# Kernel tuning notes

Measured on AMD Instinct MI355X. Metric: run time of the kernel, lower is better.

Reference implementation:

```python
import jax, jax.numpy as jnp
import numpy as np

B, L, H, F = 8, 1024, 512, 4

def setup_inputs() -> dict:
    key = jax.random.key(0)
    ks = jax.random.split(key, 5)
    x = jax.random.normal(ks[0], (B, L, H), dtype=jnp.float32)
    x_mask = jax.random.randint(ks[1], (B, L), 0, 2).astype(jnp.int32)
    W_proj = jax.random.normal(ks[2], (H, H * F), dtype=jnp.float32) * (1.0 / np.sqrt(H))
    b_proj = jnp.zeros((H * F,), dtype=jnp.float32)
    W_gate = jax.random.normal(ks[3], (2 * H, 2 * H), dtype=jnp.float32) * (1.0 / np.sqrt(2 * H))
    b_gate = jnp.zeros((2 * H,), dtype=jnp.float32)
    return {"x": x, "x_mask": x_mask, "W_proj": W_proj, "b_proj": b_proj,
            "W_gate": W_gate, "b_gate": b_gate}

def masked_softmax(logits, mask, eps=1e-13):
    # allennlp-style masked softmax used throughout sgnlp:
    # softmax(logits * mask) * mask, renormalized.
    m = mask.astype(logits.dtype)
    p = jax.nn.softmax(logits * m, axis=-1) * m
    return p / (p.sum(axis=-1, keepdims=True) + eps)

def reference(x, x_mask, W_proj, b_proj, W_gate, b_gate):
    b, l, h = x.shape
    # multi-factor projection: (B,L,H) -> (B,L,H,F) with relu (Linear activation='relu', dropout=0)
    y = jax.nn.relu(jnp.einsum('blh,hk->blk', x, W_proj) + b_proj)
    y = y.reshape(b, l, h, F)
    # per-factor self-attn scores stacked on last axis: (B,L,L,F)
    scores = jnp.einsum('blhf,bmhf->blmf', y, y)
    self_attn = scores.max(axis=-1)  # attn_pooling == 'max'
    # pairwise mask, zero diagonal
    mask = x_mask[:, :, None] * x_mask[:, None, :]
    mask = mask * (1 - jnp.eye(l, dtype=mask.dtype))
    alpha = masked_softmax(self_attn, mask)
    multi_attn_enc = jnp.einsum('blm,bmh->blh', alpha, x)
    joint = jnp.concatenate([x, multi_attn_enc], axis=-1)  # (B,L,2H)
    gate = jax.nn.sigmoid(jnp.einsum('blk,kj->blj', joint, W_gate) + b_gate)
    return gate * joint
```

## Files before the change

### kernel.cpp

```cpp
#include <hip/hip_runtime.h>


typedef _Float16 half8 __attribute__((ext_vector_type(8)));
typedef float floatx4 __attribute__((ext_vector_type(4)));

typedef const __attribute__((address_space(1))) void* gas_ptr;
typedef __attribute__((address_space(3))) void* las_ptr;


template<int NCH, int NT>
__device__ __forceinline__ void init_ptrs(const _Float16* src, int row0, int ld,
                                          const _Float16* gp[NCH]) {
  int t = threadIdx.x;
#pragma unroll
  for (int p = 0; p < NCH; ++p) {
    int c = p * NT + t;
    int row = c >> 3;
    int kg = c & 7;
    int gk = (kg ^ (row & 7)) << 3;
    gp[p] = src + (size_t)(row0 + row) * ld + gk;
  }
}

template<int NCH, int NT>
__device__ __forceinline__ void stage(const _Float16* const gp[NCH], _Float16* ldsbuf) {
  int t = threadIdx.x;
#pragma unroll
  for (int p = 0; p < NCH; ++p)
    __builtin_amdgcn_global_load_lds((gas_ptr)gp[p],
                                     (las_ptr)(ldsbuf + t * 8 + p * NT * 8), 16, 0, 0);
}

template<int NCH>
__device__ __forceinline__ void bump(const _Float16* gp[NCH], int d) {
#pragma unroll
  for (int p = 0; p < NCH; ++p) gp[p] += d;
}

__device__ __forceinline__ half8 frag_ld(const _Float16* lds, int row, int g) {
  return *(const half8*)(lds + row * 64 + ((g ^ (row & 7)) << 3));
}

__device__ __forceinline__ void mfma_tile44(const _Float16* lds_a, const _Float16* lds_b,
                                            floatx4 acc[4][4], int wm, int wn,
                                            int l16, int quad) {
#pragma unroll
  for (int kf = 0; kf < 2; ++kf) {
    half8 af[4], bf[4];
#pragma unroll
    for (int i = 0; i < 4; ++i) af[i] = frag_ld(lds_a, wm * 64 + i * 16 + l16, kf * 4 + quad);
#pragma unroll
    for (int i = 0; i < 4; ++i) bf[i] = frag_ld(lds_b, wn * 64 + i * 16 + l16, kf * 4 + quad);
#pragma unroll
    for (int mi = 0; mi < 4; ++mi)
#pragma unroll
      for (int ni = 0; ni < 4; ++ni)
        acc[mi][ni] = __builtin_amdgcn_mfma_f32_16x16x32_f16(af[mi], bf[ni], acc[mi][ni], 0, 0, 0);
  }
}

#define ZERO_ACC44(acc)                                 \
  _Pragma("unroll") for (int mi = 0; mi < 4; ++mi)      \
  _Pragma("unroll") for (int ni = 0; ni < 4; ++ni)      \
  _Pragma("unroll") for (int r = 0; r < 4; ++r) acc[mi][ni][r] = 0.0f;

__device__ __forceinline__ void mfma_tile42(const _Float16* la, const _Float16* lb,
                                            floatx4 acc[4][2], int wm, int wn,
                                            int l16, int quad) {
#pragma unroll
  for (int kf = 0; kf < 2; ++kf) {
    half8 af[4], bf[2];
#pragma unroll
    for (int i = 0; i < 4; ++i) af[i] = frag_ld(la, wm * 64 + i * 16 + l16, kf * 4 + quad);
#pragma unroll
    for (int i = 0; i < 2; ++i) bf[i] = frag_ld(lb, wn * 32 + i * 16 + l16, kf * 4 + quad);
#pragma unroll
    for (int mi = 0; mi < 4; ++mi)
#pragma unroll
      for (int ni = 0; ni < 2; ++ni)
        acc[mi][ni] = __builtin_amdgcn_mfma_f32_16x16x32_f16(af[mi], bf[ni], acc[mi][ni], 0, 0, 0);
  }
}

#define ZERO_ACC42(acc)                                 \
  _Pragma("unroll") for (int mi = 0; mi < 4; ++mi)      \
  _Pragma("unroll") for (int ni = 0; ni < 2; ++ni)      \
  _Pragma("unroll") for (int r = 0; r < 4; ++r) acc[mi][ni][r] = 0.0f;


__global__ __launch_bounds__(256) void prep_kernel(const float* __restrict__ xin,
                                                   _Float16* __restrict__ x16,
                                                   _Float16* __restrict__ xT,
                                                   const float* __restrict__ Wp,
                                                   _Float16* __restrict__ WpT,
                                                   const float* __restrict__ Wg,
                                                   _Float16* __restrict__ WgT) {
  __shared__ float tile[32][33];
  int id = blockIdx.x;
  int tx = threadIdx.x & 31, ty = threadIdx.x >> 5;
  if (id < 4096) {
    const int R = 1024, C = 512;
    int b = id & 7, rest = id >> 3;
    int c0 = (rest & 15) * 32, r0 = (rest >> 4) * 32;
    size_t boff = (size_t)b * R * C;
    const float* in = xin + boff;
    _Float16* o16 = x16 + boff;
    _Float16* oT = xT + boff;
#pragma unroll
    for (int i = 0; i < 32; i += 8) {
      float v = in[(size_t)(r0 + ty + i) * C + c0 + tx];
      tile[ty + i][tx] = v;
      o16[(size_t)(r0 + ty + i) * C + c0 + tx] = (_Float16)v;
    }
    __syncthreads();
#pragma unroll
    for (int i = 0; i < 32; i += 8)
      oT[(size_t)(c0 + ty + i) * R + r0 + tx] = (_Float16)tile[tx][ty + i];
  } else {
    int w = id - 4096;
    int bx = w & 63, by = (w >> 6) & 15, bz = w >> 10;
    const float* in; _Float16* out; int R, C, c0, r0;
    if (bz == 0) {
      in = Wp; out = WpT; R = 512; C = 2048;
      c0 = bx * 32; r0 = by * 32;
    } else {
      in = Wg; out = WgT; R = 1024; C = 1024;
      c0 = (bx & 31) * 32; r0 = (by * 2 + (bx >> 5)) * 32;
    }
#pragma unroll
    for (int i = 0; i < 32; i += 8)
      tile[ty + i][tx] = in[(size_t)(r0 + ty + i) * C + c0 + tx];
    __syncthreads();
#pragma unroll
    for (int i = 0; i < 32; i += 8) {
      int rr = c0 + ty + i;
      int prow = (bz == 0) ? ((rr & 3) * 512 + (rr >> 2)) : rr;
      out[(size_t)prow * R + r0 + tx] = (_Float16)tile[tx][ty + i];
    }
  }
}


__global__ __launch_bounds__(256) void proj_kernel(const _Float16* __restrict__ x16,
                                                   const _Float16* __restrict__ WpT,
                                                   const float* __restrict__ bp,
                                                   _Float16* __restrict__ y_t) {
  __shared__ __align__(16) _Float16 ldsA[2][128 * 64];
  __shared__ __align__(16) _Float16 ldsB[2][128 * 64];
  int i0 = blockIdx.x * 128, n0 = blockIdx.y * 128;
  int t = threadIdx.x, lane = t & 63, w = t >> 6;
  int wm = w >> 1, wn = w & 1, quad = lane >> 4, l16 = lane & 15;
  const _Float16* gpA[4]; const _Float16* gpB[4];
  init_ptrs<4, 256>(x16, i0, 512, gpA);
  init_ptrs<4, 256>(WpT, n0, 512, gpB);
  floatx4 acc[4][4];
  ZERO_ACC44(acc);
  stage<4, 256>(gpA, ldsA[0]); bump<4>(gpA, 64);
  stage<4, 256>(gpB, ldsB[0]); bump<4>(gpB, 64);
#pragma unroll 1
  for (int kt = 0; kt < 8; ++kt) {
    __syncthreads();
    if (kt < 7) {
      stage<4, 256>(gpA, ldsA[(kt + 1) & 1]); bump<4>(gpA, 64);
      stage<4, 256>(gpB, ldsB[(kt + 1) & 1]); bump<4>(gpB, 64);
    }
    mfma_tile44(ldsA[kt & 1], ldsB[kt & 1], acc, wm, wn, l16, quad);
  }
#pragma unroll
  for (int mi = 0; mi < 4; ++mi)
#pragma unroll
    for (int ni = 0; ni < 4; ++ni)
#pragma unroll
      for (int r = 0; r < 4; ++r) {
        int gr = i0 + wm * 64 + mi * 16 + quad * 4 + r;
        int gc = n0 + wn * 64 + ni * 16 + l16;
        int f = gc >> 9, h = gc & 511;
        float c = fmaxf(acc[mi][ni][r] + bp[h * 4 + f], 0.0f);
        int b = gr >> 10, l = gr & 1023;
        y_t[(((size_t)(b * 4 + f)) * 1024 + l) * 512 + h] = (_Float16)c;
      }
}


__global__ __launch_bounds__(256, 3) void score_kernel(const _Float16* __restrict__ y_t,
                                                       float* __restrict__ S) {
  __shared__ __align__(16) char smem[49152];
  _Float16* LA0 = (_Float16*)smem;
  _Float16* LA1 = (_Float16*)(smem + 16384);
  _Float16* LB0 = (_Float16*)(smem + 32768);
  _Float16* LB1 = (_Float16*)(smem + 40960);
  int id = blockIdx.x;
  int b = id & 7;
  int tt = id >> 3;
  int ti = 0;
  while (tt >= 16 - 2 * ti) { tt -= 16 - 2 * ti; ++ti; }
  int jh = 2 * ti + tt;
  int i0 = ti * 128, j0 = jh * 64;
  int t = threadIdx.x, lane = t & 63, w = t >> 6;
  int wm = w >> 1, wn = w & 1, quad = lane >> 4, l16 = lane & 15;
  const int PLANE = 1024 * 512;
  const _Float16* base = y_t + (size_t)b * 4 * PLANE;
  const _Float16* gpA[4]; const _Float16* gpB[2];
  init_ptrs<4, 256>(base, i0, 512, gpA);
  init_ptrs<2, 256>(base, j0, 512, gpB);
  floatx4 acc[4][2], smax[4][2];
  ZERO_ACC42(acc);
  stage<4, 256>(gpA, LA0); bump<4>(gpA, 64);
  stage<2, 256>(gpB, LB0); bump<2>(gpB, 64);
#pragma unroll 1
  for (int f = 0; f < 4; ++f) {
#pragma unroll 1
    for (int kt = 0; kt < 8; ++kt) {
      __syncthreads();
      if (f * 8 + kt < 31) {
        if (kt == 7) { bump<4>(gpA, PLANE - 512); bump<2>(gpB, PLANE - 512); }
        stage<4, 256>(gpA, ((kt + 1) & 1) ? LA1 : LA0); bump<4>(gpA, 64);
        stage<2, 256>(gpB, ((kt + 1) & 1) ? LB1 : LB0); bump<2>(gpB, 64);
      }
      mfma_tile42((kt & 1) ? LA1 : LA0, (kt & 1) ? LB1 : LB0, acc, wm, wn, l16, quad);
    }
    if (f == 0) {
#pragma unroll
      for (int mi = 0; mi < 4; ++mi)
#pragma unroll
        for (int ni = 0; ni < 2; ++ni) smax[mi][ni] = acc[mi][ni];
    } else {
#pragma unroll
      for (int mi = 0; mi < 4; ++mi)
#pragma unroll
        for (int ni = 0; ni < 2; ++ni)
#pragma unroll
          for (int r = 0; r < 4; ++r)
            smax[mi][ni][r] = fmaxf(smax[mi][ni][r], acc[mi][ni][r]);
    }
    ZERO_ACC42(acc);
  }
  float* Sb = S + (size_t)b * 1024 * 1024;
#pragma unroll
  for (int mi = 0; mi < 4; ++mi)
#pragma unroll
    for (int ni = 0; ni < 2; ++ni)
#pragma unroll
      for (int r = 0; r < 4; ++r) {
        int gi = i0 + wm * 64 + mi * 16 + quad * 4 + r;
        int gj = j0 + wn * 32 + ni * 16 + l16;
        Sb[(size_t)gi * 1024 + gj] = smax[mi][ni][r];
      }
  if (jh >= 2 * ti + 2) {
    __syncthreads();
    float* tl = (float*)smem;
#pragma unroll
    for (int mi = 0; mi < 4; ++mi)
#pragma unroll
      for (int ni = 0; ni < 2; ++ni)
#pragma unroll
        for (int r = 0; r < 4; ++r)
          tl[(wm * 64 + mi * 16 + quad * 4 + r) * 65 + (wn * 32 + ni * 16 + l16)] =
              smax[mi][ni][r];
    __syncthreads();
#pragma unroll 1
    for (int k = 0; k < 32; ++k) {
      int flat = k * 256 + t;
      int rm = flat >> 7, cm = flat & 127;
      Sb[(size_t)(j0 + rm) * 1024 + (i0 + cm)] = tl[cm * 65 + rm];
    }
  }
}


__global__ __launch_bounds__(256) void softmax_kernel(const float* __restrict__ S,
                                                      const int* __restrict__ xmask,
                                                      _Float16* __restrict__ alpha) {
  __shared__ float red[16];
  int row = blockIdx.x;
  int b = row >> 10, l = row & 1023;
  const float* sr = S + (size_t)row * 1024;
  const int* mr = xmask + b * 1024;
  int t = threadIdx.x, lane = t & 63, wid = t >> 6;
  int rm = mr[l];
  float v[4], mm[4];
  float vmax = 0.0f;
#pragma unroll
  for (int q = 0; q < 4; ++q) {
    int i = t + q * 256;
    int m = (rm && mr[i] && (i != l)) ? 1 : 0;
    mm[q] = (float)m;
    v[q] = m ? sr[i] : 0.0f;
    vmax = fmaxf(vmax, v[q]);
  }
  for (int off = 32; off; off >>= 1) vmax = fmaxf(vmax, __shfl_down(vmax, off));
  if (lane == 0) red[wid] = vmax;
  __syncthreads();
  if (t == 0) red[8] = fmaxf(fmaxf(red[0], red[1]), fmaxf(red[2], red[3]));
  __syncthreads();
  vmax = red[8];
  float e[4], E = 0.0f, E2 = 0.0f;
#pragma unroll
  for (int q = 0; q < 4; ++q) {
    e[q] = expf(v[q] - vmax);
    E += e[q];
    E2 += e[q] * mm[q];
  }
  for (int off = 32; off; off >>= 1) {
    E += __shfl_down(E, off);
    E2 += __shfl_down(E2, off);
  }
  if (lane == 0) { red[wid] = E; red[4 + wid] = E2; }
  __syncthreads();
  if (t == 0) {
    red[9] = red[0] + red[1] + red[2] + red[3];
    red[10] = red[4] + red[5] + red[6] + red[7];
  }
  __syncthreads();
  E = red[9]; E2 = red[10];
  float inv = 1.0f / (E2 + 1e-13f * E);
  _Float16* ar = alpha + (size_t)row * 1024;
#pragma unroll
  for (int q = 0; q < 4; ++q) {
    int i = t + q * 256;
    ar[i] = (_Float16)(e[q] * mm[q] * inv);
  }
}


__global__ __launch_bounds__(256) void attn_kernel(const _Float16* __restrict__ alpha,
                                                   const _Float16* __restrict__ xT,
                                                   _Float16* __restrict__ enc) {
  __shared__ __align__(16) _Float16 ldsA[2][64 * 64];
  __shared__ __align__(16) _Float16 ldsB[2][128 * 64];
  int id = blockIdx.x;
  int b = id & 7;
  int r2 = id >> 3;
  int i0 = (r2 >> 2) * 64;
  int n0 = (r2 & 3) * 128;
  const _Float16* A = alpha + (size_t)b * 1024 * 1024;
  const _Float16* Bm = xT + (size_t)b * 512 * 1024;
  int t = threadIdx.x, lane = t & 63, wn = t >> 6;
  int quad = lane >> 4, l16 = lane & 15;
  const _Float16* gpA[2]; const _Float16* gpB[4];
  init_ptrs<2, 256>(A, i0, 1024, gpA);
  init_ptrs<4, 256>(Bm, n0, 1024, gpB);
  floatx4 acc[4][2];
  ZERO_ACC42(acc);
  stage<2, 256>(gpA, ldsA[0]); bump<2>(gpA, 64);
  stage<4, 256>(gpB, ldsB[0]); bump<4>(gpB, 64);
#pragma unroll 1
  for (int kt = 0; kt < 16; ++kt) {
    __syncthreads();
    if (kt < 15) {
      stage<2, 256>(gpA, ldsA[(kt + 1) & 1]); bump<2>(gpA, 64);
      stage<4, 256>(gpB, ldsB[(kt + 1) & 1]); bump<4>(gpB, 64);
    }
    const _Float16* la = ldsA[kt & 1];
    const _Float16* lb = ldsB[kt & 1];
#pragma unroll
    for (int kf = 0; kf < 2; ++kf) {
      half8 af[4], bf[2];
#pragma unroll
      for (int i = 0; i < 4; ++i) af[i] = frag_ld(la, i * 16 + l16, kf * 4 + quad);
#pragma unroll
      for (int i = 0; i < 2; ++i) bf[i] = frag_ld(lb, wn * 32 + i * 16 + l16, kf * 4 + quad);
#pragma unroll
      for (int mi = 0; mi < 4; ++mi)
#pragma unroll
        for (int ni = 0; ni < 2; ++ni)
          acc[mi][ni] = __builtin_amdgcn_mfma_f32_16x16x32_f16(af[mi], bf[ni], acc[mi][ni], 0, 0, 0);
    }
  }
  _Float16* eb = enc + (size_t)b * 1024 * 512;
#pragma unroll
  for (int mi = 0; mi < 4; ++mi)
#pragma unroll
    for (int ni = 0; ni < 2; ++ni)
#pragma unroll
      for (int r = 0; r < 4; ++r) {
        int gr = i0 + mi * 16 + quad * 4 + r;
        int gc = n0 + wn * 32 + ni * 16 + l16;
        eb[(size_t)gr * 512 + gc] = (_Float16)acc[mi][ni][r];
      }
}


__global__ __launch_bounds__(256) void gate_kernel(const _Float16* __restrict__ x16,
                                                   const _Float16* __restrict__ enc,
                                                   const _Float16* __restrict__ WgT,
                                                   const float* __restrict__ bg,
                                                   float* __restrict__ out) {
  __shared__ __align__(16) _Float16 ldsA[2][128 * 64];
  __shared__ __align__(16) _Float16 ldsB[2][128 * 64];
  int i0 = blockIdx.x * 128, n0 = blockIdx.y * 128;
  int t = threadIdx.x, lane = t & 63, w = t >> 6;
  int wm = w >> 1, wn = w & 1, quad = lane >> 4, l16 = lane & 15;
  const _Float16* gpA[4]; const _Float16* gpA2[4]; const _Float16* gpB[4];
  init_ptrs<4, 256>(x16, i0, 512, gpA);
  init_ptrs<4, 256>(enc, i0, 512, gpA2);
  init_ptrs<4, 256>(WgT, n0, 1024, gpB);
  floatx4 acc[4][4];
  ZERO_ACC44(acc);
  stage<4, 256>(gpA, ldsA[0]); bump<4>(gpA, 64);
  stage<4, 256>(gpB, ldsB[0]); bump<4>(gpB, 64);
#pragma unroll 1
  for (int kt = 0; kt < 16; ++kt) {
    __syncthreads();
    if (kt < 15) {
      if (kt < 7) { stage<4, 256>(gpA,  ldsA[(kt + 1) & 1]); bump<4>(gpA, 64); }
      else        { stage<4, 256>(gpA2, ldsA[(kt + 1) & 1]); bump<4>(gpA2, 64); }
      stage<4, 256>(gpB, ldsB[(kt + 1) & 1]); bump<4>(gpB, 64);
    }
    mfma_tile44(ldsA[kt & 1], ldsB[kt & 1], acc, wm, wn, l16, quad);
  }
#pragma unroll
  for (int mi = 0; mi < 4; ++mi)
#pragma unroll
    for (int ni = 0; ni < 4; ++ni)
#pragma unroll
      for (int r = 0; r < 4; ++r) {
        int gr = i0 + wm * 64 + mi * 16 + quad * 4 + r;
        int gc = n0 + wn * 64 + ni * 16 + l16;
        float c = acc[mi][ni][r] + bg[gc];
        float g = 1.0f / (1.0f + expf(-c));
        float jv = (gc < 512) ? (float)x16[(size_t)gr * 512 + gc]
                              : (float)enc[(size_t)gr * 512 + (gc - 512)];
        out[(size_t)gr * 1024 + gc] = g * jv;
      }
}


extern "C" void kernel_launch(void* const* d_in, const int* in_sizes, int n_in,
                              void* d_out, int out_size, void* d_ws, size_t ws_size,
                              hipStream_t stream) {
  const float* x  = (const float*)d_in[0];
  const int* xm   = (const int*)d_in[1];
  const float* Wp = (const float*)d_in[2];
  const float* bp = (const float*)d_in[3];
  const float* Wg = (const float*)d_in[4];
  const float* bg = (const float*)d_in[5];
  float* out = (float*)d_out;

  char* ws = (char*)d_ws;
  const size_t MB = 1024 * 1024;
  _Float16* x16 = (_Float16*)(ws);
  _Float16* xT  = (_Float16*)(ws + 8 * MB);
  _Float16* WpT = (_Float16*)(ws + 16 * MB);
  _Float16* WgT = (_Float16*)(ws + 18 * MB);
  _Float16* y_t = (_Float16*)(ws + 20 * MB);
  float*    S   = (float*)(ws + 52 * MB);
  _Float16* alpha = (_Float16*)(ws + 20 * MB);
  _Float16* enc   = (_Float16*)(ws + 36 * MB);

  prep_kernel<<<6144, 256, 0, stream>>>(x, x16, xT, Wp, WpT, Wg, WgT);

  proj_kernel<<<dim3(64, 16), 256, 0, stream>>>(x16, WpT, bp, y_t);
  score_kernel<<<576, 256, 0, stream>>>(y_t, S);
  softmax_kernel<<<8192, 256, 0, stream>>>(S, xm, alpha);
  attn_kernel<<<512, 256, 0, stream>>>(alpha, xT, enc);
  gate_kernel<<<dim3(64, 8), 256, 0, stream>>>(x16, enc, WgT, bg, out);
}
```

Baseline: 198.9 us.

## Fuse masked softmax into attention GEMM, keeping alpha rows in LDS

Merges the softmax and attention kernels into one. Each 512-thread block computes a 32-row strip of alpha in LDS (one wave per row, wave-level reductions), then multiplies it by xT, with B fragments read directly from global memory in a register double buffer. This removes the fp16 alpha round-trip through global memory and one launch. The cost is a grid of only 256 large blocks with heavy LDS use, so occupancy is lower. B fragments are also loaded uncoalesced from global without LDS staging.

Measured after the change: 206.9 us. 1.04x slower.

```diff
diff --git a/kernel.cpp b/kernel.cpp
--- a/kernel.cpp
+++ b/kernel.cpp
@@ -2,6 +2,7 @@
 
 
 typedef _Float16 half8 __attribute__((ext_vector_type(8)));
+typedef _Float16 half4v __attribute__((ext_vector_type(4)));
 typedef float floatx4 __attribute__((ext_vector_type(4)));
 
 typedef const __attribute__((address_space(1))) void* gas_ptr;
@@ -268,114 +269,115 @@
 }
 
 
-__global__ __launch_bounds__(256) void softmax_kernel(const float* __restrict__ S,
-                                                      const int* __restrict__ xmask,
-                                                      _Float16* __restrict__ alpha) {
-  __shared__ float red[16];
-  int row = blockIdx.x;
-  int b = row >> 10, l = row & 1023;
-  const float* sr = S + (size_t)row * 1024;
-  const int* mr = xmask + b * 1024;
-  int t = threadIdx.x, lane = t & 63, wid = t >> 6;
-  int rm = mr[l];
-  float v[4], mm[4];
-  float vmax = 0.0f;
-#pragma unroll
-  for (int q = 0; q < 4; ++q) {
-    int i = t + q * 256;
-    int m = (rm && mr[i] && (i != l)) ? 1 : 0;
-    mm[q] = (float)m;
-    v[q] = m ? sr[i] : 0.0f;
-    vmax = fmaxf(vmax, v[q]);
-  }
-  for (int off = 32; off; off >>= 1) vmax = fmaxf(vmax, __shfl_down(vmax, off));
-  if (lane == 0) red[wid] = vmax;
+__global__ __launch_bounds__(512) void smattn_kernel(const float* __restrict__ S,
+                                                     const int* __restrict__ xmask,
+                                                     const _Float16* __restrict__ xT,
+                                                     _Float16* __restrict__ enc) {
+  __shared__ __align__(16) _Float16 lal[16 * 2048];
+  __shared__ float lm[1024];
+  int id = blockIdx.x;
+  int b = id & 7, it = id >> 3;
+  int i0 = it * 32;
+  int t = threadIdx.x, lane = t & 63, w = t >> 6;
+  lm[t] = (float)xmask[b * 1024 + t];
+  lm[t + 512] = (float)xmask[b * 1024 + t + 512];
   __syncthreads();
-  if (t == 0) red[8] = fmaxf(fmaxf(red[0], red[1]), fmaxf(red[2], red[3]));
+  const float* Sb = S + ((size_t)b * 1024 + i0) * 1024;
+#pragma unroll 1
+  for (int rr = 0; rr < 4; ++rr) {
+    int r = w * 4 + rr;
+    int grow = i0 + r;
+    float rmv = lm[grow];
+    const float* sr = Sb + (size_t)r * 1024;
+    float e[16], mk[16];
+    float vmax = 0.0f;
+#pragma unroll
+    for (int q = 0; q < 4; ++q) {
+      float4 sv = *(const float4*)(sr + q * 256 + lane * 4);
+#pragma unroll
+      for (int u = 0; u < 4; ++u) {
+        int j = q * 256 + lane * 4 + u;
+        float m = (rmv != 0.0f && lm[j] != 0.0f && j != grow) ? 1.0f : 0.0f;
+        float v = m * ((const float*)&sv)[u];
+        mk[q * 4 + u] = m;
+        e[q * 4 + u] = v;
+        vmax = fmaxf(vmax, v);
+      }
+    }
+#pragma unroll
+    for (int off = 32; off; off >>= 1) vmax = fmaxf(vmax, __shfl_xor(vmax, off));
+    float E = 0.0f, E2 = 0.0f;
+#pragma unroll
+    for (int i = 0; i < 16; ++i) {
+      e[i] = expf(e[i] - vmax);
+      E += e[i];
+      E2 += e[i] * mk[i];
+    }
+#pragma unroll
+    for (int off = 32; off; off >>= 1) {
+      E += __shfl_xor(E, off);
+      E2 += __shfl_xor(E2, off);
+    }
+    float inv = 1.0f / (E2 + 1e-13f * E);
+#pragma unroll
+    for (int q = 0; q < 4; ++q) {
+      int kt = q * 4 + (lane >> 4);
+      int jg = (lane >> 1) & 7;
+      int off8 = (lane & 1) * 4;
+      half4v hv;
+#pragma unroll
+      for (int u = 0; u < 4; ++u) hv[u] = (_Float16)(e[q * 4 + u] * mk[q * 4 + u] * inv);
+      *(half4v*)(&lal[kt * 2048 + r * 64 + ((jg ^ (r & 7)) << 3) + off8]) = hv;
+    }
+  }
   __syncthreads();
-  vmax = red[8];
-  float e[4], E = 0.0f, E2 = 0.0f;
-#pragma unroll
-  for (int q = 0; q < 4; ++q) {
-    e[q] = expf(v[q] - vmax);
-    E += e[q];
-    E2 += e[q] * mm[q];
-  }
-  for (int off = 32; off; off >>= 1) {
-    E += __shfl_down(E, off);
-    E2 += __shfl_down(E2, off);
-  }
-  if (lane == 0) { red[wid] = E; red[4 + wid] = E2; }
-  __syncthreads();
-  if (t == 0) {
-    red[9] = red[0] + red[1] + red[2] + red[3];
-    red[10] = red[4] + red[5] + red[6] + red[7];
-  }
-  __syncthreads();
-  E = red[9]; E2 = red[10];
-  float inv = 1.0f / (E2 + 1e-13f * E);
-  _Float16* ar = alpha + (size_t)row * 1024;
-#pragma unroll
-  for (int q = 0; q < 4; ++q) {
-    int i = t + q * 256;
-    ar[i] = (_Float16)(e[q] * mm[q] * inv);
-  }
-}
-
-
-__global__ __launch_bounds__(256) void attn_kernel(const _Float16* __restrict__ alpha,
-                                                   const _Float16* __restrict__ xT,
-                                                   _Float16* __restrict__ enc) {
-  __shared__ __align__(16) _Float16 ldsA[2][64 * 64];
-  __shared__ __align__(16) _Float16 ldsB[2][128 * 64];
-  int id = blockIdx.x;
-  int b = id & 7;
-  int r2 = id >> 3;
-  int i0 = (r2 >> 2) * 64;
-  int n0 = (r2 & 3) * 128;
-  const _Float16* A = alpha + (size_t)b * 1024 * 1024;
-  const _Float16* Bm = xT + (size_t)b * 512 * 1024;
-  int t = threadIdx.x, lane = t & 63, wn = t >> 6;
   int quad = lane >> 4, l16 = lane & 15;
-  const _Float16* gpA[2]; const _Float16* gpB[4];
-  init_ptrs<2, 256>(A, i0, 1024, gpA);
-  init_ptrs<4, 256>(Bm, n0, 1024, gpB);
-  floatx4 acc[4][2];
-  ZERO_ACC42(acc);
-  stage<2, 256>(gpA, ldsA[0]); bump<2>(gpA, 64);
-  stage<4, 256>(gpB, ldsB[0]); bump<4>(gpB, 64);
-#pragma unroll 1
-  for (int kt = 0; kt < 16; ++kt) {
-    __syncthreads();
-    if (kt < 15) {
-      stage<2, 256>(gpA, ldsA[(kt + 1) & 1]); bump<2>(gpA, 64);
-      stage<4, 256>(gpB, ldsB[(kt + 1) & 1]); bump<4>(gpB, 64);
-    }
-    const _Float16* la = ldsA[kt & 1];
-    const _Float16* lb = ldsB[kt & 1];
-#pragma unroll
-    for (int kf = 0; kf < 2; ++kf) {
-      half8 af[4], bf[2];
-#pragma unroll
-      for (int i = 0; i < 4; ++i) af[i] = frag_ld(la, i * 16 + l16, kf * 4 + quad);
-#pragma unroll
-      for (int i = 0; i < 2; ++i) bf[i] = frag_ld(lb, wn * 32 + i * 16 + l16, kf * 4 + quad);
-#pragma unroll
-      for (int mi = 0; mi < 4; ++mi)
-#pragma unroll
-        for (int ni = 0; ni < 2; ++ni)
-          acc[mi][ni] = __builtin_amdgcn_mfma_f32_16x16x32_f16(af[mi], bf[ni], acc[mi][ni], 0, 0, 0);
-    }
-  }
+  const _Float16* Bb = xT + (size_t)b * 512 * 1024;
+  floatx4 acc[2][4];
+#pragma unroll
+  for (int mi = 0; mi < 2; ++mi)
+#pragma unroll
+    for (int ni = 0; ni < 4; ++ni)
+#pragma unroll
+      for (int r = 0; r < 4; ++r) acc[mi][ni][r] = 0.0f;
+  half8 bfA[8], bfB[8];
+#define LOADB(KT, BF)                                                           \
+  _Pragma("unroll") for (int ni = 0; ni < 4; ++ni)                              \
+  _Pragma("unroll") for (int kf = 0; kf < 2; ++kf)                              \
+    BF[ni * 2 + kf] = *(const half8*)(Bb + (size_t)(w * 64 + ni * 16 + l16) * 1024 + \
+                                      (KT) * 64 + ((kf * 4 + quad) << 3));
+#define KSTEP(KT, BF)                                                           \
+  {                                                                             \
+    const _Float16* Ah = &lal[(KT) * 2048];                                     \
+    half8 af[2][2];                                                             \
+    _Pragma("unroll") for (int mi = 0; mi < 2; ++mi)                            \
+    _Pragma("unroll") for (int kf = 0; kf < 2; ++kf)                            \
+      af[mi][kf] = frag_ld(Ah, mi * 16 + l16, kf * 4 + quad);                   \
+    _Pragma("unroll") for (int mi = 0; mi < 2; ++mi)                            \
+    _Pragma("unroll") for (int ni = 0; ni < 4; ++ni)                            \
+    _Pragma("unroll") for (int kf = 0; kf < 2; ++kf)                            \
+      acc[mi][ni] = __builtin_amdgcn_mfma_f32_16x16x32_f16(af[mi][kf],          \
+          BF[ni * 2 + kf], acc[mi][ni], 0, 0, 0);                               \
+  }
+  LOADB(0, bfA);
+#pragma unroll 1
+  for (int kt = 0; kt < 16; kt += 2) {
+    LOADB(kt + 1, bfB);
+    KSTEP(kt, bfA);
+    if (kt + 2 < 16) { LOADB(kt + 2, bfA); }
+    KSTEP(kt + 1, bfB);
+  }
+#undef LOADB
+#undef KSTEP
   _Float16* eb = enc + (size_t)b * 1024 * 512;
 #pragma unroll
-  for (int mi = 0; mi < 4; ++mi)
-#pragma unroll
-    for (int ni = 0; ni < 2; ++ni)
+  for (int mi = 0; mi < 2; ++mi)
+#pragma unroll
+    for (int ni = 0; ni < 4; ++ni)
 #pragma unroll
       for (int r = 0; r < 4; ++r) {
         int gr = i0 + mi * 16 + quad * 4 + r;
-        int gc = n0 + wn * 32 + ni * 16 + l16;
+        int gc = w * 64 + ni * 16 + l16;
         eb[(size_t)gr * 512 + gc] = (_Float16)acc[mi][ni][r];
       }
 }
@@ -445,14 +447,12 @@
   _Float16* WgT = (_Float16*)(ws + 18 * MB);
   _Float16* y_t = (_Float16*)(ws + 20 * MB);
   float*    S   = (float*)(ws + 52 * MB);
-  _Float16* alpha = (_Float16*)(ws + 20 * MB);
   _Float16* enc   = (_Float16*)(ws + 36 * MB);
 
   prep_kernel<<<6144, 256, 0, stream>>>(x, x16, xT, Wp, WpT, Wg, WgT);
 
   proj_kernel<<<dim3(64, 16), 256, 0, stream>>>(x16, WpT, bp, y_t);
   score_kernel<<<576, 256, 0, stream>>>(y_t, S);
-  softmax_kernel<<<8192, 256, 0, stream>>>(S, xm, alpha);
-  attn_kernel<<<512, 256, 0, stream>>>(alpha, xT, enc);
+  smattn_kernel<<<256, 512, 0, stream>>>(S, xm, xT, enc);
   gate_kernel<<<dim3(64, 8), 256, 0, stream>>>(x16, enc, WgT, bg, out);
 }
```
